# Kernel optimization log

Hardware: AMD Instinct MI355X
Metric: run time of the kernel (lower is better)

## Reference

```python
import jax, jax.numpy as jnp
import numpy as np

CROP = 512
GRID = 8
NBINS = 256
CLIP_LIMIT = 0.8


def _clahe(x):
    # x: [B, C, H, W] in [0, 1], H and W divisible by GRID
    B, C, H, W = x.shape
    th, tw = H // GRID, W // GRID
    tp = th * tw  # pixels per tile
    # bin index of each pixel (256 uniform bins over [0, 1])
    bins = jnp.clip((x * NBINS).astype(jnp.int32), 0, NBINS - 1)
    # per-tile histograms: [B*C*GRID*GRID, tp] -> scatter-add into 256 bins
    tiles = bins.reshape(B, C, GRID, th, GRID, tw).transpose(0, 1, 2, 4, 3, 5).reshape(-1, tp)
    hist = jax.vmap(lambda b: jnp.zeros((NBINS,), jnp.float32).at[b].add(1.0))(tiles)
    # clip histogram and redistribute excess uniformly
    clip_val = max(CLIP_LIMIT * tp / NBINS, 1.0)
    clipped = jnp.minimum(hist, clip_val)
    excess = (hist - clipped).sum(-1, keepdims=True)
    hist = clipped + excess / NBINS
    # CDF -> LUT per tile, values in [0, 255]
    lut = jnp.clip(jnp.cumsum(hist, -1) * ((NBINS - 1.0) / tp), 0.0, NBINS - 1.0)
    luts = lut.reshape(B, C, GRID, GRID, NBINS)
    # bilinear interpolation between the 4 nearest tile LUTs
    ty = (jnp.arange(H, dtype=jnp.float32) + 0.5) / th - 0.5
    tx = (jnp.arange(W, dtype=jnp.float32) + 0.5) / tw - 0.5
    y0f, x0f = jnp.floor(ty), jnp.floor(tx)
    fy = (ty - y0f)[None, None, :, None]
    fx = (tx - x0f)[None, None, None, :]
    y0 = jnp.clip(y0f, 0, GRID - 1).astype(jnp.int32)
    y1 = jnp.clip(y0f + 1, 0, GRID - 1).astype(jnp.int32)
    x0 = jnp.clip(x0f, 0, GRID - 1).astype(jnp.int32)
    x1 = jnp.clip(x0f + 1, 0, GRID - 1).astype(jnp.int32)
    bi = jnp.arange(B)[:, None, None, None]
    ci = jnp.arange(C)[None, :, None, None]
    Y0 = y0[None, None, :, None]
    Y1 = y1[None, None, :, None]
    X0 = x0[None, None, None, :]
    X1 = x1[None, None, None, :]
    v00 = luts[bi, ci, Y0, X0, bins]
    v01 = luts[bi, ci, Y0, X1, bins]
    v10 = luts[bi, ci, Y1, X0, bins]
    v11 = luts[bi, ci, Y1, X1, bins]
    top = (1.0 - fx) * v00 + fx * v01
    bot = (1.0 - fx) * v10 + fx * v11
    return ((1.0 - fy) * top + fy * bot) / (NBINS - 1.0)


def _augment(x, hflip, vflip, offy, offx, apply_clahe):
    # per-sample horizontal / vertical flips
    x = jnp.where(hflip[:, None, None, None].astype(bool), x[..., ::-1], x)
    x = jnp.where(vflip[:, None, None, None].astype(bool), x[..., ::-1, :], x)
    # per-sample random 512x512 crop
    C = x.shape[1]
    crop = jax.vmap(
        lambda img, oy, ox: jax.lax.dynamic_slice(img, (0, oy, ox), (C, CROP, CROP))
    )(x, offy, offx)
    # RandomApply(CLAHE): compute for all samples, select per sample
    eq = _clahe(crop)
    return jnp.where(apply_clahe[:, None, None, None].astype(bool), eq, crop)


def setup_inputs() -> dict:
    key = jax.random.key(0)
    ks = jax.random.split(key, 6)
    B, C, H, W = 64, 1, 640, 640
    x = jax.random.uniform(ks[0], (B, C, H, W), dtype=jnp.float32)
    hflip = jax.random.randint(ks[1], (B,), 0, 2, dtype=jnp.int32)
    vflip = jax.random.randint(ks[2], (B,), 0, 2, dtype=jnp.int32)
    offy = jax.random.randint(ks[3], (B,), 0, H - CROP + 1, dtype=jnp.int32)
    offx = jax.random.randint(ks[4], (B,), 0, W - CROP + 1, dtype=jnp.int32)
    apply_clahe = jax.random.randint(ks[5], (B,), 0, 2, dtype=jnp.int32)
    return {"x": x, "hflip": hflip, "vflip": vflip, "offy": offy, "offx": offx, "apply_clahe": apply_clahe}


def reference(x, hflip, vflip, offy, offx, apply_clahe):
    return _augment(x, hflip, vflip, offy, offx, apply_clahe)
```

## Files before the change

kernel.cpp:

```cpp
#include <hip/hip_runtime.h>

#define IH 640
#define IW 640
#define CROPSZ 512
#define NGRID 8
#define TILE 64
#define NBINS 256
#define TP (TILE*TILE)
#define CLIPV 12.8f

__global__ __launch_bounds__(256) void clahe_lut_kernel(
    const float* __restrict__ x,
    const int* __restrict__ hflip, const int* __restrict__ vflip,
    const int* __restrict__ offy,  const int* __restrict__ offx,
    const int* __restrict__ apply,
    float* __restrict__ luts)
{
    const int bt = blockIdx.x;
    const int b  = bt >> 6;
    if (!apply[b]) return;
    const int tile = bt & 63;
    const int tyi = tile >> 3, txi = tile & 7;
    const int hf = hflip[b], vf = vflip[b];
    const int oy = offy[b],  ox = offx[b];

    __shared__ unsigned int hist[NBINS];
    const int t = threadIdx.x;
    hist[t] = 0u;
    __syncthreads();

    const float* __restrict__ xb = x + (size_t)b * (IH * IW);
    const int base_y = tyi * TILE, base_x = txi * TILE;

    #pragma unroll
    for (int k = 0; k < TP / 256; ++k) {
        const int p  = t + k * 256;
        const int cy = base_y + (p >> 6);
        const int cx = base_x + (p & 63);
        int iy = oy + cy; if (vf) iy = IH - 1 - iy;
        int ix = ox + cx; if (hf) ix = IW - 1 - ix;
        const float v = xb[iy * IW + ix];
        int bin = (int)(v * 256.0f);
        bin = bin < 0 ? 0 : (bin > 255 ? 255 : bin);
        atomicAdd(&hist[bin], 1u);
    }
    __syncthreads();

    const float h       = (float)hist[t];
    const float clipped = fminf(h, CLIPV);
    float ex            = h - clipped;

    const int lane = t & 63;
    const int wid  = t >> 6;

    #pragma unroll
    for (int off = 32; off > 0; off >>= 1) ex += __shfl_down(ex, off, 64);
    __shared__ float wsum[4];
    if (lane == 0) wsum[wid] = ex;
    __syncthreads();
    const float excess = wsum[0] + wsum[1] + wsum[2] + wsum[3];

    const float hv = clipped + excess * (1.0f / (float)NBINS);

    float s = hv;
    #pragma unroll
    for (int off = 1; off < 64; off <<= 1) {
        const float n = __shfl_up(s, off, 64);
        if (lane >= off) s += n;
    }
    __shared__ float wtot[4];
    if (lane == 63) wtot[wid] = s;
    __syncthreads();
    float prefix = 0.0f;
    for (int w = 0; w < wid; ++w) prefix += wtot[w];
    s += prefix;

    float lut = s * (255.0f / (float)TP);
    lut = fminf(fmaxf(lut, 0.0f), 255.0f);
    luts[(size_t)bt * NBINS + t] = lut;
}

__global__ __launch_bounds__(256) void augment_out_kernel(
    const float* __restrict__ x,
    const int* __restrict__ hflip, const int* __restrict__ vflip,
    const int* __restrict__ offy,  const int* __restrict__ offx,
    const int* __restrict__ apply,
    const float* __restrict__ luts,
    float* __restrict__ out)
{
    const int idx4 = blockIdx.x * 256 + threadIdx.x;
    const int b    = idx4 >> 16;
    const int rem  = idx4 & 65535;
    const int y    = rem >> 7;
    const int x4   = (rem & 127) << 2;

    const int hf = hflip[b], vf = vflip[b];
    const int oy = offy[b],  ox = offx[b];
    const int ap = apply[b];

    const float* __restrict__ xb = x + (size_t)b * (IH * IW);
    int iy = oy + y; if (vf) iy = IH - 1 - iy;
    const float* __restrict__ row = xb + (size_t)iy * IW;

    float v[4];
    #pragma unroll
    for (int j = 0; j < 4; ++j) {
        int ix = ox + x4 + j; if (hf) ix = IW - 1 - ix;
        v[j] = row[ix];
    }

    float4 o;
    if (ap) {
        const float tyf = (y + 0.5f) * (1.0f / TILE) - 0.5f;
        const float y0f = floorf(tyf);
        const float fy  = tyf - y0f;
        const int   y0  = max(0, min(NGRID - 1, (int)y0f));
        const int   y1  = max(0, min(NGRID - 1, (int)y0f + 1));
        const float* __restrict__ lb = luts + (size_t)b * (64 * NBINS);

        float r[4];
        #pragma unroll
        for (int j = 0; j < 4; ++j) {
            const int xx = x4 + j;
            const float txf = (xx + 0.5f) * (1.0f / TILE) - 0.5f;
            const float x0f = floorf(txf);
            const float fx  = txf - x0f;
            const int   x0  = max(0, min(NGRID - 1, (int)x0f));
            const int   x1  = max(0, min(NGRID - 1, (int)x0f + 1));

            int bin = (int)(v[j] * 256.0f);
            bin = bin < 0 ? 0 : (bin > 255 ? 255 : bin);

            const float v00 = lb[((y0 << 3) + x0) * NBINS + bin];
            const float v01 = lb[((y0 << 3) + x1) * NBINS + bin];
            const float v10 = lb[((y1 << 3) + x0) * NBINS + bin];
            const float v11 = lb[((y1 << 3) + x1) * NBINS + bin];

            const float top = (1.0f - fx) * v00 + fx * v01;
            const float bot = (1.0f - fx) * v10 + fx * v11;
            r[j] = ((1.0f - fy) * top + fy * bot) / 255.0f;
        }
        o = make_float4(r[0], r[1], r[2], r[3]);
    } else {
        o = make_float4(v[0], v[1], v[2], v[3]);
    }
    reinterpret_cast<float4*>(out)[idx4] = o;
}

extern "C" void kernel_launch(void* const* d_in, const int* in_sizes, int n_in,
                              void* d_out, int out_size, void* d_ws, size_t ws_size,
                              hipStream_t stream) {
    const float* x     = (const float*)d_in[0];
    const int*   hflip = (const int*)d_in[1];
    const int*   vflip = (const int*)d_in[2];
    const int*   offy  = (const int*)d_in[3];
    const int*   offx  = (const int*)d_in[4];
    const int*   apply = (const int*)d_in[5];
    float*       out   = (float*)d_out;
    float*       luts  = (float*)d_ws;

    hipLaunchKernelGGL(clahe_lut_kernel, dim3(64 * 64), dim3(256), 0, stream,
                       x, hflip, vflip, offy, offx, apply, luts);

    const int nthreads4 = 64 * CROPSZ * CROPSZ / 4;
    hipLaunchKernelGGL(augment_out_kernel, dim3(nthreads4 / 256), dim3(256), 0, stream,
                       x, hflip, vflip, offy, offx, apply, luts, out);
}
```

Baseline: 206.1 us.

## Vectorize crop loads, privatize per-wavefront histograms, use nontemporal output stores

Both kernels now read four contiguous input floats per vector load instead of scalar loads. Horizontal flips are handled by loading the mirrored span and reversing the lanes. The histogram kernel keeps one shared-memory histogram per wavefront and sums them afterwards, to cut atomic contention. The output kernel writes results with nontemporal stores so they do not pollute the cache. Crop offsets are arbitrary, so the vector loads may be misaligned and rely on the hardware accepting unaligned access.

```diff
diff --git a/kernel.cpp b/kernel.cpp
--- a/kernel.cpp
+++ b/kernel.cpp
@@ -8,6 +8,8 @@
 #define NBINS 256
 #define TP (TILE*TILE)
 #define CLIPV 12.8f
+
+typedef float fvec4 __attribute__((ext_vector_type(4)));
 
 __global__ __launch_bounds__(256) void clahe_lut_kernel(
     const float* __restrict__ x,
@@ -21,37 +23,41 @@
     if (!apply[b]) return;
     const int tile = bt & 63;
     const int tyi = tile >> 3, txi = tile & 7;
-    const int hf = hflip[b], vf = vflip[b];
-    const int oy = offy[b],  ox = offx[b];
 
-    __shared__ unsigned int hist[NBINS];
-    const int t = threadIdx.x;
-    hist[t] = 0u;
+    const int oy = offy[b], ox = offx[b];
+    const int by = tyi * TILE, bx = txi * TILE;
+    const int sy = vflip[b] ? (IH - TILE - oy - by) : (oy + by);
+    const int sx = hflip[b] ? (IW - TILE - ox - bx) : (ox + bx);
+
+    __shared__ unsigned int hist[4][NBINS];
+    const int t    = threadIdx.x;
+    const int lane = t & 63;
+    const int wid  = t >> 6;
+    #pragma unroll
+    for (int w = 0; w < 4; ++w) hist[w][t] = 0u;
     __syncthreads();
 
     const float* __restrict__ xb = x + (size_t)b * (IH * IW);
-    const int base_y = tyi * TILE, base_x = txi * TILE;
 
     #pragma unroll
-    for (int k = 0; k < TP / 256; ++k) {
-        const int p  = t + k * 256;
-        const int cy = base_y + (p >> 6);
-        const int cx = base_x + (p & 63);
-        int iy = oy + cy; if (vf) iy = IH - 1 - iy;
-        int ix = ox + cx; if (hf) ix = IW - 1 - ix;
-        const float v = xb[iy * IW + ix];
-        int bin = (int)(v * 256.0f);
-        bin = bin < 0 ? 0 : (bin > 255 ? 255 : bin);
-        atomicAdd(&hist[bin], 1u);
+    for (int k = 0; k < 4; ++k) {
+        const int q    = t + k * 256;
+        const int row  = q >> 4;
+        const int col4 = (q & 15) << 2;
+        const fvec4 v = *reinterpret_cast<const fvec4*>(
+                             xb + (size_t)(sy + row) * IW + sx + col4);
+        #pragma unroll
+        for (int j = 0; j < 4; ++j) {
+            int bin = (int)(v[j] * 256.0f);
+            bin = bin < 0 ? 0 : (bin > 255 ? 255 : bin);
+            atomicAdd(&hist[wid][bin], 1u);
+        }
     }
     __syncthreads();
 
-    const float h       = (float)hist[t];
+    const float h = (float)(hist[0][t] + hist[1][t] + hist[2][t] + hist[3][t]);
     const float clipped = fminf(h, CLIPV);
-    float ex            = h - clipped;
-
-    const int lane = t & 63;
-    const int wid  = t >> 6;
+    float ex = h - clipped;
 
     #pragma unroll
     for (int off = 32; off > 0; off >>= 1) ex += __shfl_down(ex, off, 64);
@@ -88,28 +94,29 @@
     const float* __restrict__ luts,
     float* __restrict__ out)
 {
-    const int idx4 = blockIdx.x * 256 + threadIdx.x;
-    const int b    = idx4 >> 16;
-    const int rem  = idx4 & 65535;
-    const int y    = rem >> 7;
-    const int x4   = (rem & 127) << 2;
+    const int bid = blockIdx.x;
+    const int b   = bid >> 8;
+    const int t   = threadIdx.x;
+    const int q   = ((bid & 255) << 8) + t;
+    const int y   = q >> 7;
+    const int x4  = (q & 127) << 2;
 
     const int hf = hflip[b], vf = vflip[b];
     const int oy = offy[b],  ox = offx[b];
     const int ap = apply[b];
 
-    const float* __restrict__ xb = x + (size_t)b * (IH * IW);
-    int iy = oy + y; if (vf) iy = IH - 1 - iy;
-    const float* __restrict__ row = xb + (size_t)iy * IW;
+    const int iy = vf ? (IH - 1 - oy - y) : (oy + y);
+    const float* __restrict__ row = x + (size_t)b * (IH * IW) + (size_t)iy * IW;
 
-    float v[4];
-    #pragma unroll
-    for (int j = 0; j < 4; ++j) {
-        int ix = ox + x4 + j; if (hf) ix = IW - 1 - ix;
-        v[j] = row[ix];
+    fvec4 v;
+    if (hf) {
+        const fvec4 r = *reinterpret_cast<const fvec4*>(row + (IW - 4 - ox - x4));
+        v = (fvec4){r.w, r.z, r.y, r.x};
+    } else {
+        v = *reinterpret_cast<const fvec4*>(row + ox + x4);
     }
 
-    float4 o;
+    fvec4 o;
     if (ap) {
         const float tyf = (y + 0.5f) * (1.0f / TILE) - 0.5f;
         const float y0f = floorf(tyf);
@@ -118,7 +125,6 @@
         const int   y1  = max(0, min(NGRID - 1, (int)y0f + 1));
         const float* __restrict__ lb = luts + (size_t)b * (64 * NBINS);
 
-        float r[4];
         #pragma unroll
         for (int j = 0; j < 4; ++j) {
             const int xx = x4 + j;
@@ -138,13 +144,12 @@
 
             const float top = (1.0f - fx) * v00 + fx * v01;
             const float bot = (1.0f - fx) * v10 + fx * v11;
-            r[j] = ((1.0f - fy) * top + fy * bot) / 255.0f;
+            o[j] = ((1.0f - fy) * top + fy * bot) * (1.0f / 255.0f);
         }
-        o = make_float4(r[0], r[1], r[2], r[3]);
     } else {
-        o = make_float4(v[0], v[1], v[2], v[3]);
+        o = v;
     }
-    reinterpret_cast<float4*>(out)[idx4] = o;
+    __builtin_nontemporal_store(o, reinterpret_cast<fvec4*>(out) + ((size_t)bid * 256 + t));
 }
 
 extern "C" void kernel_launch(void* const* d_in, const int* in_sizes, int n_in,
@@ -162,7 +167,7 @@
     hipLaunchKernelGGL(clahe_lut_kernel, dim3(64 * 64), dim3(256), 0, stream,
                        x, hflip, vflip, offy, offx, apply, luts);
 
-    const int nthreads4 = 64 * CROPSZ * CROPSZ / 4;
-    hipLaunchKernelGGL(augment_out_kernel, dim3(nthreads4 / 256), dim3(256), 0, stream,
+    const int nblocks = 64 * (CROPSZ * CROPSZ / 4) / 256;
+    hipLaunchKernelGGL(augment_out_kernel, dim3(nblocks), dim3(256), 0, stream,
                        x, hflip, vflip, offy, offx, apply, luts, out);
 }
```

New measurement: 193.7 us. 1.06x faster.
